# Kernel tuning notes

Hardware: AMD Instinct MI355X
Metric: run time of the kernel (lower is better)

The kernel has to match this reference:

```python
import jax, jax.numpy as jnp
import numpy as np

HID = 7168; H = 128; DQ = 1536; DKV = 512; DH = 128; DR = 64; MAXS = 4096

def _rope_tables(seq_len):
    inv_freq = 1.0 / (10000.0 ** (jnp.arange(0, DR, 2, dtype=jnp.float32) / DR))
    t = jnp.arange(seq_len, dtype=jnp.float32)
    freqs = jnp.outer(t, inv_freq)              # [S, DR/2]
    emb = jnp.concatenate([freqs, freqs], -1)   # [S, DR]
    return jnp.cos(emb), jnp.sin(emb)

def _apply_rope(x, cos, sin):
    # x: [..., S, DR]; cos/sin: [S, DR]
    d = x.shape[-1]
    x1, x2 = x[..., : d // 2], x[..., d // 2 :]
    rotated = jnp.concatenate([-x2, x1], -1)
    return (x * cos + rotated * sin).astype(x.dtype)

def setup_inputs() -> dict:
    key = jax.random.key(0)
    ks = jax.random.split(key, 16)
    s = 0.02
    inp = {
        "h":    jax.random.normal(ks[0], (1, 1024, HID), jnp.float32),
        "Wdq":  jax.random.normal(ks[1], (DQ, HID), jnp.float32) * s,
        "bdq":  jnp.zeros((DQ,), jnp.float32),
        "Wdkv": jax.random.normal(ks[2], (DKV, HID), jnp.float32) * s,
        "bdkv": jnp.zeros((DKV,), jnp.float32),
        "Wuq":  jax.random.normal(ks[3], (H * DH, DQ), jnp.float32) * s,
        "buq":  jnp.zeros((H * DH,), jnp.float32),
        "Wukv": jax.random.normal(ks[4], (H * DH * 2, DKV), jnp.float32) * s,
        "bukv": jnp.zeros((H * DH * 2,), jnp.float32),
        "Wrq":  jax.random.normal(ks[5], (H * DR, DQ), jnp.float32) * s,
        "brq":  jnp.zeros((H * DR,), jnp.float32),
        "Wrk":  jax.random.normal(ks[6], (DR, HID), jnp.float32) * s,
        "brk":  jnp.zeros((DR,), jnp.float32),
        "Wo":   jax.random.normal(ks[7], (HID, H * DH), jnp.float32) * s,
        "bo":   jnp.zeros((HID,), jnp.float32),
    }
    return inp

def reference(h, Wdq, bdq, Wdkv, bdkv, Wuq, buq, Wukv, bukv, Wrq, brq, Wrk, brk, Wo, bo):
    B, S, _ = h.shape
    c_q = h @ Wdq.T + bdq              # [B,S,DQ]
    c_kv = h @ Wdkv.T + bdkv           # [B,S,DKV]
    q_c = (c_q @ Wuq.T + buq).reshape(B, S, H, DH).transpose(0, 2, 1, 3)     # [B,H,S,DH]
    kv_c = (c_kv @ Wukv.T + bukv).reshape(B, S, H, 2 * DH).transpose(0, 2, 1, 3)
    k_c, v = kv_c[..., :DH], kv_c[..., DH:]                                  # [B,H,S,DH]
    q_r = (c_q @ Wrq.T + brq).reshape(B, S, H, DR).transpose(0, 2, 1, 3)     # [B,H,S,DR]
    k_r = (h @ Wrk.T + brk).reshape(B, S, 1, DR).transpose(0, 2, 1, 3)       # [B,1,S,DR]
    cos, sin = _rope_tables(S)
    q_r = _apply_rope(q_r, cos, sin)
    k_r = _apply_rope(k_r, cos, sin)
    q = jnp.concatenate([q_c, q_r], -1)                                      # [B,H,S,DH+DR]
    k = jnp.concatenate([k_c, jnp.broadcast_to(k_r, (B, H, S, DR))], -1)
    scale = 1.0 / jnp.sqrt(jnp.float32(DH + DR))
    scores = jnp.einsum('bhqd,bhkd->bhqk', q, k) * scale
    attn = jax.nn.softmax(scores, axis=-1)
    o = jnp.einsum('bhqk,bhkd->bhqd', attn, v)        # [B,H,S,DH]
    o = o.transpose(0, 2, 1, 3).reshape(B, S, H * DH)
    return o @ Wo.T + bo
```

## Files before the change

### kernel.cpp

```cpp
#include <hip/hip_runtime.h>
#include <hip/hip_bf16.h>

#define S_LEN 1024
#define HID 7168
#define NH 128
#define DQ 1536
#define DKV 512
#define DH 128
#define DR 64

typedef __attribute__((ext_vector_type(8))) short bf16x8;
typedef __attribute__((ext_vector_type(4))) float f32x4;
typedef __attribute__((ext_vector_type(4))) float fl4;
typedef __attribute__((ext_vector_type(4))) unsigned short us4;
typedef __attribute__((ext_vector_type(8))) unsigned short us8;
typedef __attribute__((ext_vector_type(4))) unsigned int u32x4;

static __device__ __forceinline__ unsigned short f2bf(float f) {
  union { float f; unsigned int u; } v; v.f = f;
  unsigned int u = v.u;
  return (unsigned short)((u + 0x7fffu + ((u >> 16) & 1u)) >> 16);
}
static __device__ __forceinline__ float bf2f(unsigned short u) {
  union { unsigned int u; float f; } v; v.u = ((unsigned int)u) << 16;
  return v.f;
}
static __device__ __forceinline__ unsigned int cvtpk2(float lo, float hi) {
  unsigned int r;
  asm("v_cvt_pk_bf16_f32 %0, %1, %2" : "=v"(r) : "v"(lo), "v"(hi));
  return r;
}

__global__ __launch_bounds__(256) void cvt_bf16_kernel(
    const float* __restrict__ in, unsigned short* __restrict__ out, int n8) {
  int i = blockIdx.x * 256 + threadIdx.x;
  int stride = gridDim.x * 256;
  for (; i < n8; i += stride) {
    fl4 a = ((const fl4*)in)[2 * i];
    fl4 b = ((const fl4*)in)[2 * i + 1];
    us8 u = { f2bf(a[0]), f2bf(a[1]), f2bf(a[2]), f2bf(a[3]),
              f2bf(b[0]), f2bf(b[1]), f2bf(b[2]), f2bf(b[3]) };
    ((us8*)out)[i] = u;
  }
}

template <int OUTMODE, int WFP32, int ROPEQ = 0>
__global__ __launch_bounds__(256) void gemm_k(
    const unsigned short* __restrict__ A, int lda,
    const unsigned short* __restrict__ Wb16,
    const float* __restrict__ Wfa, const float* __restrict__ Wfb, int nsplit,
    int ldw,
    const float* __restrict__ bias,
    void* __restrict__ Cv, int ldc, size_t zstride,
    int Ncl, int ksl, float alpha,
    const float* __restrict__ ctab = nullptr,
    const float* __restrict__ stab = nullptr)
{
  const int n0 = blockIdx.x * 128;
  if (n0 >= Ncl) return;

  __shared__ unsigned short As[128 * 64];
  __shared__ unsigned short Ws[128 * 64];
  const int t = threadIdx.x;
  const int l = t & 63, w = t >> 6;
  const int r15 = l & 15, g = l >> 4;
  const int wm = (w >> 1) * 64, wn = (w & 1) * 64;
  const int m0 = blockIdx.y * 128;
  const int kbase = blockIdx.z * ksl;
  const int srow = l >> 3;
  const int scol = (l & 7) * 8;

  f32x4 acc[4][4];
#pragma unroll
  for (int i = 0; i < 4; ++i)
#pragma unroll
    for (int j = 0; j < 4; ++j) acc[i][j] = (f32x4){0.f, 0.f, 0.f, 0.f};

  const unsigned short* Ab = A + (size_t)m0 * lda;
  const unsigned short* Wb = nullptr;
  const float* Wf = nullptr;
  if constexpr (WFP32) {
    Wf = (n0 < nsplit) ? Wfa + (size_t)n0 * ldw : Wfb + (size_t)(n0 - nsplit) * ldw;
  } else {
    Wb = Wb16 + (size_t)n0 * ldw;
  }

  fl4 wx[4], wy[4];
  auto issueW = [&](int k0) {
#pragma unroll
    for (int i = 0; i < 4; ++i) {
      int c = t + 256 * i;
      const float* src = Wf + (size_t)(c >> 3) * ldw + k0 + (c & 7) * 8;
      wx[i] = *(const fl4*)src;
      wy[i] = *(const fl4*)(src + 4);
    }
  };

  if constexpr (WFP32) issueW(kbase);
  const int kend = kbase + ksl;

  for (int k0 = kbase; k0 < kend; k0 += 64) {
    if constexpr (WFP32) {
      __builtin_amdgcn_s_barrier();
      __builtin_amdgcn_sched_barrier(0);
    } else {
      __syncthreads();
    }
#pragma unroll
    for (int i = 0; i < 4; ++i) {
      int chunk = w * 4 + i;
      int row = chunk * 8 + srow;
      __builtin_amdgcn_global_load_lds(
          (const __attribute__((address_space(1))) void*)(Ab + (size_t)row * lda + k0 + scol),
          (__attribute__((address_space(3))) void*)(As + chunk * 512), 16, 0, 0);
      if constexpr (!WFP32) {
        __builtin_amdgcn_global_load_lds(
            (const __attribute__((address_space(1))) void*)(Wb + (size_t)row * ldw + k0 + scol),
            (__attribute__((address_space(3))) void*)(Ws + chunk * 512), 16, 0, 0);
      }
    }
    if constexpr (WFP32) {
      __builtin_amdgcn_sched_barrier(0);
      asm volatile("s_waitcnt vmcnt(4)" ::: "memory");
      __builtin_amdgcn_sched_barrier(0);
#pragma unroll
      for (int i = 0; i < 4; ++i) {
        int c = t + 256 * i;
        u32x4 p = { cvtpk2(wx[i][0], wx[i][1]), cvtpk2(wx[i][2], wx[i][3]),
                    cvtpk2(wy[i][0], wy[i][1]), cvtpk2(wy[i][2], wy[i][3]) };
        ((u32x4*)Ws)[c] = p;
      }
      if (k0 + 64 < kend) {
        issueW(k0 + 64);
        __builtin_amdgcn_sched_barrier(0);
        asm volatile("s_waitcnt vmcnt(8) lgkmcnt(0)" ::: "memory");
      } else {
        asm volatile("s_waitcnt vmcnt(0) lgkmcnt(0)" ::: "memory");
      }
      __builtin_amdgcn_sched_barrier(0);
      __builtin_amdgcn_s_barrier();
    } else {
      __syncthreads();
    }
#pragma unroll
    for (int kk = 0; kk < 2; ++kk) {
      bf16x8 a[4], b[4];
#pragma unroll
      for (int mt = 0; mt < 4; ++mt)
        a[mt] = *reinterpret_cast<const bf16x8*>(&As[(wm + mt * 16 + r15) * 64 + kk * 32 + 8 * g]);
#pragma unroll
      for (int nt = 0; nt < 4; ++nt)
        b[nt] = *reinterpret_cast<const bf16x8*>(&Ws[(wn + nt * 16 + r15) * 64 + kk * 32 + 8 * g]);
#pragma unroll
      for (int mt = 0; mt < 4; ++mt)
#pragma unroll
        for (int nt = 0; nt < 4; ++nt)
          acc[mt][nt] = __builtin_amdgcn_mfma_f32_16x16x32_bf16(a[mt], b[nt], acc[mt][nt], 0, 0, 0);
    }
  }

  if constexpr (OUTMODE == 1) {
    float bv[4];
#pragma unroll
    for (int nt = 0; nt < 4; ++nt) {
      int col = n0 + wn + nt * 16 + r15;
      bv[nt] = (col < Ncl) ? bias[col] : 0.f;
    }
    bool isrope = false;
    if constexpr (ROPEQ) isrope = (n0 + wn) >= 16384;
    if (ROPEQ && isrope) {
#pragma unroll
      for (int mt = 0; mt < 4; ++mt)
#pragma unroll
        for (int r = 0; r < 4; ++r) {
          int row = m0 + wm + mt * 16 + g * 4 + r;
#pragma unroll
          for (int ntp = 0; ntp < 2; ++ntp) {
            int j = ntp * 16 + r15;
            float c = ctab[row * 32 + j];
            float s = stab[row * 32 + j];
            float x1 = acc[mt][ntp][r] + bv[ntp];
            float x2 = acc[mt][ntp + 2][r] + bv[ntp + 2];
            int col1 = n0 + wn + ntp * 16 + r15;
            ((unsigned short*)Cv)[(size_t)row * ldc + col1] =
                f2bf((x1 * c - x2 * s) * alpha);
            ((unsigned short*)Cv)[(size_t)row * ldc + col1 + 32] =
                f2bf((x2 * c + x1 * s) * alpha);
          }
        }
    } else {
#pragma unroll
      for (int mt = 0; mt < 4; ++mt)
#pragma unroll
        for (int nt = 0; nt < 4; ++nt) {
          int col = n0 + wn + nt * 16 + r15;
          if (col < Ncl) {
#pragma unroll
            for (int r = 0; r < 4; ++r) {
              int row = m0 + wm + mt * 16 + g * 4 + r;
              ((unsigned short*)Cv)[(size_t)row * ldc + col] =
                  f2bf((acc[mt][nt][r] + bv[nt]) * alpha);
            }
          }
        }
    }
  } else {
    float* Cp = (float*)Cv + blockIdx.z * zstride;
#pragma unroll
    for (int mt = 0; mt < 4; ++mt)
#pragma unroll
      for (int nt = 0; nt < 4; ++nt) {
        int col = n0 + wn + nt * 16 + r15;
        if (col < Ncl) {
#pragma unroll
          for (int r = 0; r < 4; ++r) {
            int row = m0 + wm + mt * 16 + g * 4 + r;
            Cp[(size_t)row * ldc + col] = acc[mt][nt][r];
          }
        }
      }
  }
}

__global__ __launch_bounds__(256) void gemm_g4(
    const unsigned short* __restrict__ A,
    const float* __restrict__ W,
    float* __restrict__ pbuf)
{
  __shared__ unsigned short As[128 * 64];
  __shared__ unsigned short Ws[128 * 64];
  const int t = threadIdx.x;
  const int l = t & 63, w = t >> 6;
  const int r15 = l & 15, g = l >> 4;
  const int wm = (w >> 1) * 64, wn = (w & 1) * 64;
  const int bid = blockIdx.x;
  const int z = bid / 448;
  const int r448 = bid % 448;
  const int grp = r448 >> 6, wi = r448 & 63;
  const int m0 = (wi >> 3) * 128;
  const int n0 = (grp * 8 + (wi & 7)) * 128;
  const int kbase = z * 8192;
  const int srow = l >> 3, scol = (l & 7) * 8;

  f32x4 acc[4][4];
#pragma unroll
  for (int i = 0; i < 4; ++i)
#pragma unroll
    for (int j = 0; j < 4; ++j) acc[i][j] = (f32x4){0.f, 0.f, 0.f, 0.f};

  const unsigned short* Ab = A + (size_t)m0 * 16384;
  const float* Wf = W + (size_t)n0 * 16384;

  fl4 wx[4], wy[4];
  auto issueW = [&](int k0) {
#pragma unroll
    for (int i = 0; i < 4; ++i) {
      int c = t + 256 * i;
      const float* src = Wf + (size_t)(c >> 3) * 16384 + k0 + (c & 7) * 8;
      wx[i] = *(const fl4*)src;
      wy[i] = *(const fl4*)(src + 4);
    }
  };
  issueW(kbase);
  const int kend = kbase + 8192;

  for (int k0 = kbase; k0 < kend; k0 += 64) {
    __builtin_amdgcn_s_barrier();
    __builtin_amdgcn_sched_barrier(0);
#pragma unroll
    for (int i = 0; i < 4; ++i) {
      int chunk = w * 4 + i;
      int row = chunk * 8 + srow;
      __builtin_amdgcn_global_load_lds(
          (const __attribute__((address_space(1))) void*)(Ab + (size_t)row * 16384 + k0 + scol),
          (__attribute__((address_space(3))) void*)(As + chunk * 512), 16, 0, 0);
    }
    __builtin_amdgcn_sched_barrier(0);
    asm volatile("s_waitcnt vmcnt(4)" ::: "memory");
    __builtin_amdgcn_sched_barrier(0);
#pragma unroll
    for (int i = 0; i < 4; ++i) {
      int c = t + 256 * i;
      u32x4 p = { cvtpk2(wx[i][0], wx[i][1]), cvtpk2(wx[i][2], wx[i][3]),
                  cvtpk2(wy[i][0], wy[i][1]), cvtpk2(wy[i][2], wy[i][3]) };
      ((u32x4*)Ws)[c] = p;
    }
    if (k0 + 64 < kend) {
      issueW(k0 + 64);
      __builtin_amdgcn_sched_barrier(0);
      asm volatile("s_waitcnt vmcnt(8) lgkmcnt(0)" ::: "memory");
    } else {
      asm volatile("s_waitcnt vmcnt(0) lgkmcnt(0)" ::: "memory");
    }
    __builtin_amdgcn_sched_barrier(0);
    __builtin_amdgcn_s_barrier();
#pragma unroll
    for (int kk = 0; kk < 2; ++kk) {
      bf16x8 a[4], b[4];
#pragma unroll
      for (int mt = 0; mt < 4; ++mt)
        a[mt] = *reinterpret_cast<const bf16x8*>(&As[(wm + mt * 16 + r15) * 64 + kk * 32 + 8 * g]);
#pragma unroll
      for (int nt = 0; nt < 4; ++nt)
        b[nt] = *reinterpret_cast<const bf16x8*>(&Ws[(wn + nt * 16 + r15) * 64 + kk * 32 + 8 * g]);
#pragma unroll
      for (int mt = 0; mt < 4; ++mt)
#pragma unroll
        for (int nt = 0; nt < 4; ++nt)
          acc[mt][nt] = __builtin_amdgcn_mfma_f32_16x16x32_bf16(a[mt], b[nt], acc[mt][nt], 0, 0, 0);
    }
  }

  float* Cp = pbuf + (size_t)z * 1024 * 7168;
#pragma unroll
  for (int mt = 0; mt < 4; ++mt)
#pragma unroll
    for (int nt = 0; nt < 4; ++nt) {
      int col = n0 + wn + nt * 16 + r15;
#pragma unroll
      for (int r = 0; r < 4; ++r) {
        int row = m0 + wm + mt * 16 + g * 4 + r;
        Cp[(size_t)row * 7168 + col] = acc[mt][nt][r];
      }
    }
}

__global__ __launch_bounds__(256) void reduce_f32_kernel(
    const float* __restrict__ pbuf, const float* __restrict__ bias,
    float* __restrict__ out, int ldo, int rowlen4, int nz, size_t zstride, int total4)
{
  int idx = blockIdx.x * 256 + threadIdx.x;
  if (idx >= total4) return;
  int r = idx / rowlen4, c4 = idx % rowlen4;
  fl4 acc = *(const fl4*)(bias + c4 * 4);
  for (int z = 0; z < nz; ++z)
    acc += *(const fl4*)(pbuf + z * zstride + (size_t)idx * 4);
  *(fl4*)(out + (size_t)r * ldo + c4 * 4) = acc;
}

__global__ __launch_bounds__(256) void reduce_bf16_kernel(
    const float* __restrict__ pbuf, const float* __restrict__ bias,
    unsigned short* __restrict__ out, int ldo, int rowlen4, int nz, size_t zstride, int total4)
{
  int idx = blockIdx.x * 256 + threadIdx.x;
  if (idx >= total4) return;
  int r = idx / rowlen4, c4 = idx % rowlen4;
  fl4 acc = *(const fl4*)(bias + c4 * 4);
  for (int z = 0; z < nz; ++z)
    acc += *(const fl4*)(pbuf + z * zstride + (size_t)idx * 4);
  us4 u = { f2bf(acc[0]), f2bf(acc[1]), f2bf(acc[2]), f2bf(acc[3]) };
  *(us4*)(out + (size_t)r * ldo + c4 * 4) = u;
}

__global__ __launch_bounds__(256) void rope_table_kernel(float* __restrict__ ctab,
                                                         float* __restrict__ stab) {
  int idx = blockIdx.x * 256 + threadIdx.x;
  if (idx >= S_LEN * 32) return;
  int j = idx & 31, s = idx >> 5;
  float invf = expf(-0.28782313662425574f * (float)j);
  float ang = (float)s * invf;
  ctab[idx] = cosf(ang);
  stab[idx] = sinf(ang);
}

__global__ void rope_bf16_kernel(unsigned short* __restrict__ x, int nh, int lda, int total,
                                 const float* __restrict__ ctab,
                                 const float* __restrict__ stab) {
  int idx = blockIdx.x * 256 + threadIdx.x;
  if (idx >= total) return;
  int j = idx & 31;
  int rest = idx >> 5;
  int hh = rest % nh;
  int s = rest / nh;
  float c = ctab[s * 32 + j], sn = stab[s * 32 + j];
  size_t base = (size_t)s * lda + hh * 64;
  float x1 = bf2f(x[base + j]), x2 = bf2f(x[base + j + 32]);
  x[base + j]      = f2bf(x1 * c - x2 * sn);
  x[base + j + 32] = f2bf(x2 * c + x1 * sn);
}

__global__ __launch_bounds__(256) void vtrans_kernel(
    const unsigned short* __restrict__ kvb, unsigned short* __restrict__ vt) {
  __shared__ unsigned short tl[64][72];
  const int s0 = blockIdx.x * 64;
  const int c0 = blockIdx.y * 64;
  const int t = threadIdx.x;
  const int rr = t >> 3, cc = (t & 7) * 8;
  const int hbase = (c0 >> 7) * 256 + 128 + (c0 & 127);
#pragma unroll
  for (int i = 0; i < 2; ++i) {
    int r = rr + i * 32;
    *reinterpret_cast<bf16x8*>(&tl[r][cc]) =
        *reinterpret_cast<const bf16x8*>(kvb + (size_t)(s0 + r) * 32768 + hbase + cc);
  }
  __syncthreads();
#pragma unroll
  for (int i = 0; i < 2; ++i) {
    int vc = rr + i * 32;
    unsigned short tmp[8];
#pragma unroll
    for (int j = 0; j < 8; ++j) tmp[j] = tl[cc + j][vc];
    *reinterpret_cast<bf16x8*>(&vt[(size_t)(c0 + vc) * 1024 + s0 + cc]) =
        *reinterpret_cast<bf16x8*>(tmp);
  }
}

__global__ __launch_bounds__(512) void mla_attn_kernel(
    const unsigned short* __restrict__ qcat,
    const unsigned short* __restrict__ kvb,
    const unsigned short* __restrict__ kr,
    const unsigned short* __restrict__ vt,
    unsigned short* __restrict__ obuf)
{
  __shared__ unsigned short Klds[64][200];
  __shared__ unsigned short Vlds[128][72];
  __shared__ unsigned short Plds[8][16][72];

  const int t = threadIdx.x;
  const int l = t & 63, w = t >> 6;
  const int r15 = l & 15, g = l >> 4;
  const int bid = blockIdx.x;
  const int orig = (bid & 7) * 128 + (bid >> 3);
  const int h = orig >> 3;
  const int q0 = (orig & 7) * 128;

  bf16x8 qf[6];
  const unsigned short* qrow = qcat + (size_t)(q0 + w * 16 + r15) * 24576;
#pragma unroll
  for (int kk = 0; kk < 4; ++kk)
    qf[kk] = *reinterpret_cast<const bf16x8*>(qrow + h * 128 + kk * 32 + 8 * g);
#pragma unroll
  for (int kk = 4; kk < 6; ++kk)
    qf[kk] = *reinterpret_cast<const bf16x8*>(qrow + 16384 + h * 64 + (kk - 4) * 32 + 8 * g);

  bf16x8 kreg[3], vreg[2];
  auto loadKV = [&](int kk0) {
#pragma unroll
    for (int i = 0; i < 3; ++i) {
      int c = t + 512 * i, row = c / 24, cb = c % 24;
      const unsigned short* src = (cb < 16)
          ? kvb + (size_t)(kk0 + row) * 32768 + h * 256 + cb * 8
          : kr + (size_t)(kk0 + row) * 2112 + (cb - 16) * 8;
      kreg[i] = *reinterpret_cast<const bf16x8*>(src);
    }
#pragma unroll
    for (int i = 0; i < 2; ++i) {
      int c = t + 512 * i, d = c >> 3, kb = c & 7;
      vreg[i] = *reinterpret_cast<const bf16x8*>(vt + ((size_t)h * 128 + d) * 1024 + kk0 + kb * 8);
    }
  };

  float m_r[4], l_r[4];
  f32x4 oacc[8];
#pragma unroll
  for (int r = 0; r < 4; ++r) { m_r[r] = -1e30f; l_r[r] = 0.f; }
#pragma unroll
  for (int d = 0; d < 8; ++d) oacc[d] = (f32x4){0.f, 0.f, 0.f, 0.f};

  loadKV(0);

  for (int kt = 0; kt < 16; ++kt) {
    __syncthreads();
#pragma unroll
    for (int i = 0; i < 3; ++i) {
      int c = t + 512 * i, row = c / 24, cb = c % 24;
      *reinterpret_cast<bf16x8*>(&Klds[row][cb * 8]) = kreg[i];
    }
#pragma unroll
    for (int i = 0; i < 2; ++i) {
      int c = t + 512 * i, d = c >> 3, kb = c & 7;
      *reinterpret_cast<bf16x8*>(&Vlds[d][kb * 8]) = vreg[i];
    }
    __syncthreads();
    if (kt < 15) loadKV((kt + 1) * 64);

    f32x4 sacc[4];
#pragma unroll
    for (int nt = 0; nt < 4; ++nt) sacc[nt] = (f32x4){0.f, 0.f, 0.f, 0.f};
    __builtin_amdgcn_s_setprio(1);
#pragma unroll
    for (int nt = 0; nt < 4; ++nt)
#pragma unroll
      for (int kk = 0; kk < 6; ++kk) {
        bf16x8 b = *reinterpret_cast<const bf16x8*>(&Klds[nt * 16 + r15][kk * 32 + 8 * g]);
        sacc[nt] = __builtin_amdgcn_mfma_f32_16x16x32_bf16(qf[kk], b, sacc[nt], 0, 0, 0);
      }
    __builtin_amdgcn_s_setprio(0);

    float sc[4], rsum[4];
#pragma unroll
    for (int r = 0; r < 4; ++r) {
      float mx = fmaxf(fmaxf(sacc[0][r], sacc[1][r]), fmaxf(sacc[2][r], sacc[3][r]));
      mx = fmaxf(mx, __shfl_xor(mx, 1));
      mx = fmaxf(mx, __shfl_xor(mx, 2));
      mx = fmaxf(mx, __shfl_xor(mx, 4));
      mx = fmaxf(mx, __shfl_xor(mx, 8));
      float mn = fmaxf(m_r[r], mx);
      sc[r] = __expf(m_r[r] - mn);
      m_r[r] = mn;
      rsum[r] = 0.f;
    }
#pragma unroll
    for (int nt = 0; nt < 4; ++nt)
#pragma unroll
      for (int r = 0; r < 4; ++r) {
        float p = __expf(sacc[nt][r] - m_r[r]);
        rsum[r] += p;
        Plds[w][g * 4 + r][nt * 16 + r15] = f2bf(p);
      }
#pragma unroll
    for (int r = 0; r < 4; ++r) {
      float s = rsum[r];
      s += __shfl_xor(s, 1);
      s += __shfl_xor(s, 2);
      s += __shfl_xor(s, 4);
      s += __shfl_xor(s, 8);
      l_r[r] = l_r[r] * sc[r] + s;
    }
#pragma unroll
    for (int d = 0; d < 8; ++d)
#pragma unroll
      for (int r = 0; r < 4; ++r) oacc[d][r] *= sc[r];

    bf16x8 pa0 = *reinterpret_cast<const bf16x8*>(&Plds[w][r15][8 * g]);
    bf16x8 pa1 = *reinterpret_cast<const bf16x8*>(&Plds[w][r15][32 + 8 * g]);
    __builtin_amdgcn_s_setprio(1);
#pragma unroll
    for (int dt = 0; dt < 8; ++dt) {
      bf16x8 v0 = *reinterpret_cast<const bf16x8*>(&Vlds[dt * 16 + r15][8 * g]);
      bf16x8 v1 = *reinterpret_cast<const bf16x8*>(&Vlds[dt * 16 + r15][32 + 8 * g]);
      oacc[dt] = __builtin_amdgcn_mfma_f32_16x16x32_bf16(pa0, v0, oacc[dt], 0, 0, 0);
      oacc[dt] = __builtin_amdgcn_mfma_f32_16x16x32_bf16(pa1, v1, oacc[dt], 0, 0, 0);
    }
    __builtin_amdgcn_s_setprio(0);
  }

#pragma unroll
  for (int dt = 0; dt < 8; ++dt)
#pragma unroll
    for (int r = 0; r < 4; ++r) {
      int row = q0 + w * 16 + g * 4 + r;
      int col = h * DH + dt * 16 + r15;
      obuf[(size_t)row * 16384 + col] = f2bf(oacc[dt][r] / l_r[r]);
    }
}

extern "C" void kernel_launch(void* const* d_in, const int* in_sizes, int n_in,
                              void* d_out, int out_size, void* d_ws, size_t ws_size,
                              hipStream_t stream) {
  const float* h    = (const float*)d_in[0];
  const float* Wdq  = (const float*)d_in[1];
  const float* bdq  = (const float*)d_in[2];
  const float* Wdkv = (const float*)d_in[3];
  const float* bdkv = (const float*)d_in[4];
  const float* Wuq  = (const float*)d_in[5];
  const float* buq  = (const float*)d_in[6];
  const float* Wukv = (const float*)d_in[7];
  const float* bukv = (const float*)d_in[8];
  const float* Wrq  = (const float*)d_in[9];
  const float* brq  = (const float*)d_in[10];
  const float* Wrk  = (const float*)d_in[11];
  const float* brk  = (const float*)d_in[12];
  const float* Wo   = (const float*)d_in[13];
  const float* bo   = (const float*)d_in[14];
  float* out = (float*)d_out;

  char* ws = (char*)d_ws;
  size_t off = 0;
  auto alloc = [&](size_t bytes) {
    char* p = ws + off;
    off += (bytes + 255) & ~(size_t)255;
    return p;
  };
  unsigned short* hb    = (unsigned short*)alloc((size_t)1024 * 7168 * 2);
  unsigned short* W1cat = (unsigned short*)alloc((size_t)2176 * 7168 * 2);
  float*          b1cat = (float*)alloc(2176 * 4);
  float*          b2cat = (float*)alloc(24576 * 4);
  unsigned short* ccat  = (unsigned short*)alloc((size_t)1024 * 2112 * 2);
  unsigned short* qcat  = (unsigned short*)alloc((size_t)1024 * 24576 * 2);
  unsigned short* kvbb  = (unsigned short*)alloc((size_t)1024 * 32768 * 2);
  unsigned short* vt    = (unsigned short*)alloc((size_t)16384 * 1024 * 2);
  unsigned short* obuf  = (unsigned short*)alloc((size_t)1024 * 16384 * 2);
  float*          ctab  = (float*)alloc((size_t)S_LEN * 32 * 4);
  float*          stab  = (float*)alloc((size_t)S_LEN * 32 * 4);
  float* pbufG1 = (float*)qcat;
  float* pbufG4 = (float*)(ws + ((size_t)544 << 20));

  auto cvt = [&](const float* in, unsigned short* outp, size_t n) {
    int n8 = (int)(n / 8);
    int blocks = (n8 + 255) / 256;
    if (blocks > 2048) blocks = 2048;
    cvt_bf16_kernel<<<blocks, 256, 0, stream>>>(in, outp, n8);
  };

  cvt(h,    hb,    (size_t)1024 * 7168);
  cvt(Wdq,  W1cat, (size_t)1536 * 7168);
  cvt(Wdkv, W1cat + (size_t)1536 * 7168, (size_t)512 * 7168);
  cvt(Wrk,  W1cat + (size_t)2048 * 7168, (size_t)64 * 7168);
  hipMemsetAsync(W1cat + (size_t)2112 * 7168, 0, (size_t)64 * 7168 * 2, stream);
  hipMemcpyAsync(b1cat,        bdq,  1536 * 4, hipMemcpyDeviceToDevice, stream);
  hipMemcpyAsync(b1cat + 1536, bdkv, 512 * 4,  hipMemcpyDeviceToDevice, stream);
  hipMemcpyAsync(b1cat + 2048, brk,  64 * 4,   hipMemcpyDeviceToDevice, stream);
  hipMemsetAsync(b1cat + 2112, 0, 64 * 4, stream);
  hipMemcpyAsync(b2cat,         buq, 16384 * 4, hipMemcpyDeviceToDevice, stream);
  hipMemcpyAsync(b2cat + 16384, brq, 8192 * 4,  hipMemcpyDeviceToDevice, stream);
  rope_table_kernel<<<(S_LEN * 32 + 255) / 256, 256, 0, stream>>>(ctab, stab);

  const float scale = 0.07216878364870323f;
  const int BIGN = 1 << 30;
  dim3 blk(256);

  gemm_k<2, 0><<<dim3(24, 8, 4), blk, 0, stream>>>(
      hb, 7168, W1cat, nullptr, nullptr, BIGN, 7168, nullptr,
      pbufG1, 2112, (size_t)1024 * 2112, 2112, 1792, 1.0f);
  reduce_bf16_kernel<<<2112, blk, 0, stream>>>(pbufG1, b1cat, ccat, 2112, 528, 4,
                                               (size_t)1024 * 2112, 1024 * 2112 / 4);
  rope_bf16_kernel<<<(1024 * 32 + 255) / 256, blk, 0, stream>>>(ccat + 2048, 1, 2112, 1024 * 32, ctab, stab);

  gemm_k<1, 1, 1><<<dim3(192, 8, 1), blk, 0, stream>>>(
      ccat, 2112, nullptr, Wuq, Wrq, 16384, 1536, b2cat,
      qcat, 24576, 0, 24576, 1536, scale, ctab, stab);

  gemm_k<1, 1><<<dim3(256, 8, 1), blk, 0, stream>>>(
      ccat + 1536, 2112, nullptr, Wukv, Wukv, BIGN, 512, bukv,
      kvbb, 32768, 0, 32768, 512, 1.0f);
  vtrans_kernel<<<dim3(16, 256), blk, 0, stream>>>(kvbb, vt);
  mla_attn_kernel<<<dim3(1024), dim3(512), 0, stream>>>(qcat, kvbb, ccat + 2048, vt, obuf);

  gemm_g4<<<dim3(896), blk, 0, stream>>>(obuf, Wo, pbufG4);
  reduce_f32_kernel<<<7168, blk, 0, stream>>>(pbufG4, bo, out,
                                              7168, 1792, 2, (size_t)1024 * 7168, 1024 * 7168 / 4);
}
```

Baseline: 1.122 ms.

## Rewrite output projection GEMM as 256x256 eight-phase ping-pong kernel on bf16 Wo

Replaces the Wo projection GEMM with a 512-thread kernel. Each block computes a 256x256 output tile and double-buffers 64-wide K slices in 128KB of LDS with XOR-swizzled reads. The loop interleaves LDS reads, async global-to-LDS staging and MFMA bursts in eight barrier-separated phases, raising wave priority during MFMA. Wo is now converted to bf16 by a separate pass on every call, instead of being converted from fp32 inside the GEMM's inner loop. Split-K goes from 2 to 8, so the final reduction sums eight partial buffers, which adds partial-sum write and read traffic and an extra full pass over Wo.

```diff
diff --git a/kernel.cpp b/kernel.cpp
--- a/kernel.cpp
+++ b/kernel.cpp
@@ -222,107 +222,167 @@
   }
 }
 
-__global__ __launch_bounds__(256) void gemm_g4(
+#define G4_DSREAD_A(buf, mh)                                                  \
+  _Pragma("unroll") for (int mf = 0; mf < 4; ++mf)                            \
+  _Pragma("unroll") for (int kk = 0; kk < 2; ++kk)                            \
+    af[mf][kk] = rdA(buf, mh, mf, kk);
+
+#define G4_DSREAD_B(buf, nh, breg)                                            \
+  _Pragma("unroll") for (int nf = 0; nf < 2; ++nf)                            \
+  _Pragma("unroll") for (int kk = 0; kk < 2; ++kk)                            \
+    breg[nf][kk] = rdB(buf, nh, nf, kk);
+
+#define G4_MFMA(mh, nh, breg)                                                 \
+  __builtin_amdgcn_s_setprio(1);                                              \
+  _Pragma("unroll") for (int kk = 0; kk < 2; ++kk)                            \
+  _Pragma("unroll") for (int mf = 0; mf < 4; ++mf)                            \
+  _Pragma("unroll") for (int nf = 0; nf < 2; ++nf)                            \
+    acc[mh][nh][mf][nf] = __builtin_amdgcn_mfma_f32_16x16x32_bf16(            \
+        af[mf][kk], breg[nf][kk], acc[mh][nh][mf][nf], 0, 0, 0);              \
+  __builtin_amdgcn_s_setprio(0);
+
+#define G4_BAR_IN()                                                           \
+  __builtin_amdgcn_s_barrier();                                               \
+  asm volatile("s_waitcnt lgkmcnt(0)" ::: "memory");                          \
+  __builtin_amdgcn_sched_barrier(0);
+
+#define G4_BAR_OUT()                                                          \
+  __builtin_amdgcn_sched_barrier(0);                                          \
+  __builtin_amdgcn_s_barrier();
+
+__global__ __launch_bounds__(512, 2) void gemm_g4_8ph(
     const unsigned short* __restrict__ A,
-    const float* __restrict__ W,
+    const unsigned short* __restrict__ W,
     float* __restrict__ pbuf)
 {
-  __shared__ unsigned short As[128 * 64];
-  __shared__ unsigned short Ws[128 * 64];
+  __shared__ unsigned short S[65536];
   const int t = threadIdx.x;
   const int l = t & 63, w = t >> 6;
   const int r15 = l & 15, g = l >> 4;
-  const int wm = (w >> 1) * 64, wn = (w & 1) * 64;
-  const int bid = blockIdx.x;
-  const int z = bid / 448;
-  const int r448 = bid % 448;
-  const int grp = r448 >> 6, wi = r448 & 63;
-  const int m0 = (wi >> 3) * 128;
-  const int n0 = (grp * 8 + (wi & 7)) * 128;
-  const int kbase = z * 8192;
-  const int srow = l >> 3, scol = (l & 7) * 8;
-
-  f32x4 acc[4][4];
-#pragma unroll
-  for (int i = 0; i < 4; ++i)
-#pragma unroll
-    for (int j = 0; j < 4; ++j) acc[i][j] = (f32x4){0.f, 0.f, 0.f, 0.f};
-
-  const unsigned short* Ab = A + (size_t)m0 * 16384;
-  const float* Wf = W + (size_t)n0 * 16384;
-
-  fl4 wx[4], wy[4];
-  auto issueW = [&](int k0) {
-#pragma unroll
-    for (int i = 0; i < 4; ++i) {
-      int c = t + 256 * i;
-      const float* src = Wf + (size_t)(c >> 3) * 16384 + k0 + (c & 7) * 8;
-      wx[i] = *(const fl4*)src;
-      wy[i] = *(const fl4*)(src + 4);
+  const int n0 = blockIdx.x * 256;
+  const int m0 = blockIdx.y * 256;
+  const int kbase = blockIdx.z * 2048;
+  const int NT = 32;
+
+  const int lp = l ^ (((l >> 5) & 1) << 1);
+  const int srow = lp >> 3;
+  const int scol = (lp & 7) * 8;
+  const int pr = (w >> 2) * 64;
+  const int pc = (w & 3) * 32;
+
+  f32x4 acc[2][2][4][2];
+#pragma unroll
+  for (int a0 = 0; a0 < 2; ++a0)
+#pragma unroll
+    for (int a1 = 0; a1 < 2; ++a1)
+#pragma unroll
+      for (int a2 = 0; a2 < 4; ++a2)
+#pragma unroll
+        for (int a3 = 0; a3 < 2; ++a3)
+          acc[a0][a1][a2][a3] = (f32x4){0.f, 0.f, 0.f, 0.f};
+
+  auto stage = [&](int tile, int which) {
+    if (tile >= NT) return;
+    const int k0 = kbase + tile * 64;
+    const unsigned short* gb = (which < 2)
+        ? A + (size_t)(m0 + which * 128) * 16384 + k0
+        : W + (size_t)(n0 + (which - 2) * 128) * 16384 + k0;
+    unsigned short* dst = S + (tile & 1) * 32768 + which * 8192;
+#pragma unroll
+    for (int i = 0; i < 2; ++i) {
+      __builtin_amdgcn_global_load_lds(
+          (const __attribute__((address_space(1))) void*)(gb + (size_t)((w * 2 + i) * 8 + srow) * 16384 + scol),
+          (__attribute__((address_space(3))) void*)(dst + (w * 2 + i) * 512 + l * 8), 16, 0, 0);
     }
   };
-  issueW(kbase);
-  const int kend = kbase + 8192;
-
-  for (int k0 = kbase; k0 < kend; k0 += 64) {
-    __builtin_amdgcn_s_barrier();
-    __builtin_amdgcn_sched_barrier(0);
-#pragma unroll
-    for (int i = 0; i < 4; ++i) {
-      int chunk = w * 4 + i;
-      int row = chunk * 8 + srow;
-      __builtin_amdgcn_global_load_lds(
-          (const __attribute__((address_space(1))) void*)(Ab + (size_t)row * 16384 + k0 + scol),
-          (__attribute__((address_space(3))) void*)(As + chunk * 512), 16, 0, 0);
-    }
-    __builtin_amdgcn_sched_barrier(0);
-    asm volatile("s_waitcnt vmcnt(4)" ::: "memory");
-    __builtin_amdgcn_sched_barrier(0);
-#pragma unroll
-    for (int i = 0; i < 4; ++i) {
-      int c = t + 256 * i;
-      u32x4 p = { cvtpk2(wx[i][0], wx[i][1]), cvtpk2(wx[i][2], wx[i][3]),
-                  cvtpk2(wy[i][0], wy[i][1]), cvtpk2(wy[i][2], wy[i][3]) };
-      ((u32x4*)Ws)[c] = p;
-    }
-    if (k0 + 64 < kend) {
-      issueW(k0 + 64);
-      __builtin_amdgcn_sched_barrier(0);
-      asm volatile("s_waitcnt vmcnt(8) lgkmcnt(0)" ::: "memory");
-    } else {
-      asm volatile("s_waitcnt vmcnt(0) lgkmcnt(0)" ::: "memory");
-    }
-    __builtin_amdgcn_sched_barrier(0);
-    __builtin_amdgcn_s_barrier();
-#pragma unroll
-    for (int kk = 0; kk < 2; ++kk) {
-      bf16x8 a[4], b[4];
-#pragma unroll
-      for (int mt = 0; mt < 4; ++mt)
-        a[mt] = *reinterpret_cast<const bf16x8*>(&As[(wm + mt * 16 + r15) * 64 + kk * 32 + 8 * g]);
-#pragma unroll
-      for (int nt = 0; nt < 4; ++nt)
-        b[nt] = *reinterpret_cast<const bf16x8*>(&Ws[(wn + nt * 16 + r15) * 64 + kk * 32 + 8 * g]);
-#pragma unroll
-      for (int mt = 0; mt < 4; ++mt)
-#pragma unroll
-        for (int nt = 0; nt < 4; ++nt)
-          acc[mt][nt] = __builtin_amdgcn_mfma_f32_16x16x32_bf16(a[mt], b[nt], acc[mt][nt], 0, 0, 0);
-    }
-  }
-
-  float* Cp = pbuf + (size_t)z * 1024 * 7168;
-#pragma unroll
-  for (int mt = 0; mt < 4; ++mt)
-#pragma unroll
-    for (int nt = 0; nt < 4; ++nt) {
-      int col = n0 + wn + nt * 16 + r15;
-#pragma unroll
-      for (int r = 0; r < 4; ++r) {
-        int row = m0 + wm + mt * 16 + g * 4 + r;
-        Cp[(size_t)row * 7168 + col] = acc[mt][nt][r];
-      }
-    }
+
+  auto rdA = [&](int buf, int mh, int mf, int kk) -> bf16x8 {
+    int row = pr + mf * 16 + r15;
+    int L = row * 128 + kk * 64 + g * 16;
+    L ^= ((L >> 9) & 1) << 5;
+    return *(const bf16x8*)((const char*)S + buf * 65536 + mh * 16384 + L);
+  };
+  auto rdB = [&](int buf, int nh, int nf, int kk) -> bf16x8 {
+    int row = pc + nf * 16 + r15;
+    int L = row * 128 + kk * 64 + g * 16;
+    L ^= ((L >> 9) & 1) << 5;
+    return *(const bf16x8*)((const char*)S + buf * 65536 + (2 + nh) * 16384 + L);
+  };
+
+  bf16x8 af[4][2], bA[2][2], bB[2][2];
+
+  stage(0, 0); stage(0, 1); stage(0, 2); stage(0, 3);
+  stage(1, 0); stage(1, 2); stage(1, 3);
+  __builtin_amdgcn_sched_barrier(0);
+  asm volatile("s_waitcnt vmcnt(6)" ::: "memory");
+  __builtin_amdgcn_sched_barrier(0);
+  __builtin_amdgcn_s_barrier();
+
+  for (int i = 0; i < 16; ++i) {
+    const int tb = 2 * i;
+    const bool last = (i == 15);
+    G4_DSREAD_A(0, 0)
+    G4_DSREAD_B(0, 0, bA)
+    stage(tb + 1, 1);
+    G4_BAR_IN()
+    G4_MFMA(0, 0, bA)
+    G4_BAR_OUT()
+    G4_DSREAD_B(0, 1, bB)
+    stage(tb + 2, 0);
+    G4_BAR_IN()
+    G4_MFMA(0, 1, bB)
+    G4_BAR_OUT()
+    G4_DSREAD_A(0, 1)
+    stage(tb + 2, 2);
+    G4_BAR_IN()
+    G4_MFMA(1, 1, bB)
+    G4_BAR_OUT()
+    stage(tb + 2, 3);
+    G4_BAR_IN()
+    G4_MFMA(1, 0, bA)
+    if (last) { asm volatile("s_waitcnt vmcnt(0)" ::: "memory"); }
+    else      { asm volatile("s_waitcnt vmcnt(6)" ::: "memory"); }
+    G4_BAR_OUT()
+    G4_DSREAD_A(1, 0)
+    G4_DSREAD_B(1, 0, bA)
+    stage(tb + 2, 1);
+    G4_BAR_IN()
+    G4_MFMA(0, 0, bA)
+    G4_BAR_OUT()
+    G4_DSREAD_B(1, 1, bB)
+    stage(tb + 3, 0);
+    G4_BAR_IN()
+    G4_MFMA(0, 1, bB)
+    G4_BAR_OUT()
+    G4_DSREAD_A(1, 1)
+    stage(tb + 3, 2);
+    G4_BAR_IN()
+    G4_MFMA(1, 1, bB)
+    G4_BAR_OUT()
+    stage(tb + 3, 3);
+    G4_BAR_IN()
+    G4_MFMA(1, 0, bA)
+    if (last) { asm volatile("s_waitcnt vmcnt(0)" ::: "memory"); }
+    else      { asm volatile("s_waitcnt vmcnt(6)" ::: "memory"); }
+    G4_BAR_OUT()
+  }
+
+  float* Cp = pbuf + (size_t)blockIdx.z * 1024 * 7168;
+#pragma unroll
+  for (int mh = 0; mh < 2; ++mh)
+#pragma unroll
+    for (int nh = 0; nh < 2; ++nh)
+#pragma unroll
+      for (int mf = 0; mf < 4; ++mf)
+#pragma unroll
+        for (int nf = 0; nf < 2; ++nf) {
+          int col = n0 + nh * 128 + pc + nf * 16 + r15;
+#pragma unroll
+          for (int r = 0; r < 4; ++r) {
+            int row = m0 + mh * 128 + pr + mf * 16 + g * 4 + r;
+            Cp[(size_t)row * 7168 + col] = acc[mh][nh][mf][nf][r];
+          }
+        }
 }
 
 __global__ __launch_bounds__(256) void reduce_f32_kernel(
@@ -584,7 +644,8 @@
   float*          ctab  = (float*)alloc((size_t)S_LEN * 32 * 4);
   float*          stab  = (float*)alloc((size_t)S_LEN * 32 * 4);
   float* pbufG1 = (float*)qcat;
-  float* pbufG4 = (float*)(ws + ((size_t)544 << 20));
+  unsigned short* Wob    = (unsigned short*)(ws + ((size_t)288 << 20));
+  float*          pbufG4 = (float*)(ws + ((size_t)544 << 20));
 
   auto cvt = [&](const float* in, unsigned short* outp, size_t n) {
     int n8 = (int)(n / 8);
@@ -627,7 +688,8 @@
   vtrans_kernel<<<dim3(16, 256), blk, 0, stream>>>(kvbb, vt);
   mla_attn_kernel<<<dim3(1024), dim3(512), 0, stream>>>(qcat, kvbb, ccat + 2048, vt, obuf);
 
-  gemm_g4<<<dim3(896), blk, 0, stream>>>(obuf, Wo, pbufG4);
+  cvt(Wo, Wob, (size_t)7168 * 16384);
+  gemm_g4_8ph<<<dim3(28, 4, 8), dim3(512), 0, stream>>>(obuf, Wob, pbufG4);
   reduce_f32_kernel<<<7168, blk, 0, stream>>>(pbufG4, bo, out,
-                                              7168, 1792, 2, (size_t)1024 * 7168, 1024 * 7168 / 4);
-}
+                                              7168, 1792, 8, (size_t)1024 * 7168, 1024 * 7168 / 4);
+}
```

New measurement: 1.054 ms. 1.07x faster.
